# Kernel optimization log

Measured on AMD Instinct MI355X. Metric: run time of the kernel, lower is better.

Reference implementation:

```python
import jax, jax.numpy as jnp
import numpy as np

B, N = 128, 2048
DX = 10.0 / 2048.0   # X / N
DT = 5.0e-4          # CFL-consistent timestep


def f_real(u):
    # f(u) = 0.5*u*(3 - u^2) + (300/12)*u^2*(3/4 - 2u + 3/2 u^2 - 1/4 u^4)
    u2 = u * u
    return 0.5 * u * (3.0 - u2) + 25.0 * u2 * (0.75 - 2.0 * u + 1.5 * u2 - 0.25 * u2 * u2)


def dfdu_abs(u):
    # f_real is elementwise, so grad of the sum gives the elementwise derivative,
    # matching torch.autograd.grad(f, u, grad_outputs=ones_like(f))
    return jnp.abs(jax.grad(lambda uu: jnp.sum(f_real(uu)))(u))


def setup_inputs() -> dict:
    key = jax.random.key(0)
    init = jax.random.uniform(key, (B, N), dtype=jnp.float32)  # u in [0,1]
    return {"init": init, "stepnum": 500}


def reference(init, stepnum):
    lam = jnp.float32(DT / DX)

    def step(u_old, _):
        f = f_real(u_old)                      # [B, N]
        a = dfdu_abs(u_old)                    # |f'(u)|, [B, N]
        # local Lax-Friedrichs flux: max over the (j, j+1) pair
        alpha = jnp.maximum(a[:, :-1], a[:, 1:])  # [B, N-1]
        f_half = 0.5 * (f[:, :-1] + f[:, 1:]) - 0.5 * alpha * (u_old[:, 1:] - u_old[:, :-1])
        interior = u_old[:, 1:-1] - lam * (f_half[:, 1:] - f_half[:, :-1])  # [B, N-2]
        # boundary: u[:,0]=u[:,1], u[:,N-1]=u[:,N-2]
        u = jnp.concatenate([interior[:, :1], interior, interior[:, -1:]], axis=1)
        return u, u

    _, traj = jax.lax.scan(step, init, None, length=stepnum - 1)  # [stepnum-1, B, N]
    return jnp.concatenate([init[None], traj], axis=0)            # [stepnum, B, N]
```

## Files before the change

kernel.cpp:

```cpp
#include <hip/hip_runtime.h>

#define NPTS 2048
#define TPB  768
#define CAP  1536

typedef float v2f __attribute__((ext_vector_type(2)));

#define EDGE_BARRIER() do {                                   \
    asm volatile("s_waitcnt lgkmcnt(0)" ::: "memory");        \
    __builtin_amdgcn_s_barrier();                             \
    asm volatile("" ::: "memory");                            \
} while (0)

__device__ __forceinline__ v2f s2(float x) { v2f v; v.x = x; v.y = x; return v; }

__device__ __forceinline__ v2f fma2(v2f a, v2f b, v2f c) {
#if __has_builtin(__builtin_elementwise_fma)
    return __builtin_elementwise_fma(a, b, c);
#else
    v2f r; r.x = fmaf(a.x, b.x, c.x); r.y = fmaf(a.y, b.y, c.y); return r;
#endif
}

__device__ __forceinline__ void eval_gp2(v2f u, v2f& g, v2f& p) {
    const v2f uu = u * u;
    v2f gg = fma2(uu, s2(-3.125f), s2(18.75f));
    gg = fma2(u, gg, s2(-25.25f));
    gg = fma2(u, gg, s2(9.375f));
    gg = fma2(u, gg, s2(0.75f));
    g = u * gg;
    v2f pp = fma2(uu, s2(-37.5f), s2(150.0f));
    pp = fma2(u, pp, s2(-151.5f));
    pp = fma2(u, pp, s2(37.5f));
    p = fma2(u, pp, s2(1.5f));
}

__global__ __launch_bounds__(TPB) void lxf_split(
    const float* __restrict__ init, float* __restrict__ out,
    int nbatch, int nsteps)
{
    __shared__ float UL[2][TPB];
    __shared__ float UR[2][TPB];

    const int blk = blockIdx.x;
    const int r   = blk >> 1;
    const int h   = blk & 1;
    const int tid = threadIdx.x;
    const int c0  = 2 * tid;
    const int gb  = h ? 512 : 0;
    const size_t rowoff = (size_t)r * NPTS;
    const float lam = 0.1024f;

    const bool st  = h ? (c0 >= 512) : (c0 < 1024);
    const bool bcL = (h == 0) && (tid == 0);
    const bool bcR = (h == 1) && (tid == TPB - 1);
    const int  tl  = (tid == 0)       ? 0   : tid - 1;
    const int  tr  = (tid == TPB - 1) ? tid : tid + 1;
    const int dist = h ? (509 - c0) : (c0 - 1025);

    v2f uv = *reinterpret_cast<const v2f*>(init + rowoff + gb + c0);
    v2f gv, pv;
    eval_gp2(uv, gv, pv);

    if (st) *reinterpret_cast<v2f*>(out + rowoff + gb + c0) = uv;

    UL[0][tid] = uv.x;
    UR[0][tid] = uv.y;
    EDGE_BARRIER();

    const size_t stride = (size_t)nbatch * NPTS;
    float* dstw = out + rowoff + gb + c0;

#define STEP(CUR, NXT) do {                                              \
    dstw += stride;                                                      \
    if (dist <= rem) {                                                   \
        v2f h2; h2.x = UR[CUR][tl]; h2.y = UL[CUR][tr];      \
        v2f gh, ph;                                                      \
        eval_gp2(h2, gh, ph);                                            \
        const float aL = fmaxf(fabsf(ph.x), fabsf(pv.x));                \
        const float aM = fmaxf(fabsf(pv.x), fabsf(pv.y));                \
        const float aR = fmaxf(fabsf(pv.y), fabsf(ph.y));                \
        const float fhL = fmaf(-0.5f * aL, uv.x - h2.x, gh.x + gv.x);    \
        const float fhM = fmaf(-0.5f * aM, uv.y - uv.x, gv.x + gv.y);    \
        const float fhR = fmaf(-0.5f * aR, h2.y - uv.y, gv.y + gh.y);    \
        float n0 = fmaf(-lam, fhM - fhL, uv.x);                          \
        float n1 = fmaf(-lam, fhR - fhM, uv.y);                          \
        if (bcL) n0 = n1;                           \
        if (bcR) n1 = n0;                           \
        uv.x = n0; uv.y = n1;                                            \
        eval_gp2(uv, gv, pv);                                            \
        UL[NXT][tid] = n0;                                               \
        UR[NXT][tid] = n1;                                               \
        if (st) *reinterpret_cast<v2f*>(dstw) = uv;                      \
    }                                                                    \
    --rem;                                                               \
    EDGE_BARRIER();                                                      \
} while (0)

    const int S  = nsteps - 1;
    int rem = S - 1;
    const int P2 = S >> 1;
    for (int i = 0; i < P2; ++i) {
        STEP(0, 1);
        STEP(1, 0);
    }
    if (S & 1) STEP(0, 1);
#undef STEP
}

extern "C" void kernel_launch(void* const* d_in, const int* in_sizes, int n_in,
                              void* d_out, int out_size, void* d_ws, size_t ws_size,
                              hipStream_t stream) {
    const float* init = (const float*)d_in[0];
    float* out = (float*)d_out;

    const int nbatch = in_sizes[0] / NPTS;
    const int nsteps = out_size / in_sizes[0];

    hipLaunchKernelGGL(lxf_split, dim3(2 * nbatch), dim3(TPB), 0, stream,
                       init, out, nbatch, nsteps);
}
```

Baseline: 177.8 us.

## Fuse two time steps per barrier using halo-of-two and shared f/f' values

Each thread now reads a two-point halo from both neighbours and advances two time steps per barrier, halving the number of block-wide barriers. Neighbours' f and |f'| values are shared through LDS alongside u, so halo cells are not re-evaluated. The cost is redundant recomputation of the intermediate step at the halo, three times the LDS traffic, and more registers per thread. Boundary handling for the intermediate step, and a tail for odd step counts, are added.

```diff
diff --git a/kernel.cpp b/kernel.cpp
--- a/kernel.cpp
+++ b/kernel.cpp
@@ -2,7 +2,6 @@
 
 #define NPTS 2048
 #define TPB  768
-#define CAP  1536
 
 typedef float v2f __attribute__((ext_vector_type(2)));
 
@@ -39,8 +38,9 @@
     const float* __restrict__ init, float* __restrict__ out,
     int nbatch, int nsteps)
 {
-    __shared__ float UL[2][TPB];
-    __shared__ float UR[2][TPB];
+    __shared__ v2f Us[2][TPB];
+    __shared__ v2f Gs[2][TPB];
+    __shared__ v2f Ps[2][TPB];
 
     const int blk = blockIdx.x;
     const int r   = blk >> 1;
@@ -64,48 +64,95 @@
 
     if (st) *reinterpret_cast<v2f*>(out + rowoff + gb + c0) = uv;
 
-    UL[0][tid] = uv.x;
-    UR[0][tid] = uv.y;
+    Us[0][tid] = uv; Gs[0][tid] = gv; Ps[0][tid] = pv;
     EDGE_BARRIER();
 
     const size_t stride = (size_t)nbatch * NPTS;
     float* dstw = out + rowoff + gb + c0;
 
-#define STEP(CUR, NXT) do {                                              \
-    dstw += stride;                                                      \
-    if (dist <= rem) {                                                   \
-        v2f h2; h2.x = UR[CUR][tl]; h2.y = UL[CUR][tr];      \
-        v2f gh, ph;                                                      \
-        eval_gp2(h2, gh, ph);                                            \
-        const float aL = fmaxf(fabsf(ph.x), fabsf(pv.x));                \
-        const float aM = fmaxf(fabsf(pv.x), fabsf(pv.y));                \
-        const float aR = fmaxf(fabsf(pv.y), fabsf(ph.y));                \
-        const float fhL = fmaf(-0.5f * aL, uv.x - h2.x, gh.x + gv.x);    \
-        const float fhM = fmaf(-0.5f * aM, uv.y - uv.x, gv.x + gv.y);    \
-        const float fhR = fmaf(-0.5f * aR, h2.y - uv.y, gv.y + gh.y);    \
-        float n0 = fmaf(-lam, fhM - fhL, uv.x);                          \
-        float n1 = fmaf(-lam, fhR - fhM, uv.y);                          \
-        if (bcL) n0 = n1;                           \
-        if (bcR) n1 = n0;                           \
-        uv.x = n0; uv.y = n1;                                            \
-        eval_gp2(uv, gv, pv);                                            \
-        UL[NXT][tid] = n0;                                               \
-        UR[NXT][tid] = n1;                                               \
-        if (st) *reinterpret_cast<v2f*>(dstw) = uv;                      \
-    }                                                                    \
-    --rem;                                                               \
-    EDGE_BARRIER();                                                      \
+#define FLUX(gl, gr, pl, pr, ul, ur) \
+    fmaf(-0.5f * fmaxf(fabsf(pl), fabsf(pr)), (ur) - (ul), (gl) + (gr))
+
+#define SUPER(CUR, NXT) do {                                               \
+    dstw += 2 * stride;                                                    \
+    if (dist <= rem) {                                                     \
+        const v2f uLp = Us[CUR][tl], gLp = Gs[CUR][tl], pLp = Ps[CUR][tl]; \
+        const v2f uRp = Us[CUR][tr], gRp = Gs[CUR][tr], pRp = Ps[CUR][tr]; \
+        float yu[6], yg[6], yp[6];                                         \
+        yu[0]=uLp.x; yu[1]=uLp.y; yu[2]=uv.x; yu[3]=uv.y; yu[4]=uRp.x; yu[5]=uRp.y; \
+        yg[0]=gLp.x; yg[1]=gLp.y; yg[2]=gv.x; yg[3]=gv.y; yg[4]=gRp.x; yg[5]=gRp.y; \
+        yp[0]=pLp.x; yp[1]=pLp.y; yp[2]=pv.x; yp[3]=pv.y; yp[4]=pRp.x; yp[5]=pRp.y; \
+        if (tid == 0) {                                                    \
+            yu[0]=uv.x; yu[1]=uv.x; yg[0]=gv.x; yg[1]=gv.x;                \
+            yp[0]=pv.x; yp[1]=pv.x;                                        \
+        }                                                                  \
+        if (tid == TPB - 1) {                                              \
+            yu[4]=uv.y; yu[5]=uv.y; yg[4]=gv.y; yg[5]=gv.y;                \
+            yp[4]=pv.y; yp[5]=pv.y;                                        \
+        }                                                                  \
+                                    \
+        float F[5];                                                        \
+        _Pragma("unroll")                                                  \
+        for (int j = 0; j < 5; ++j)                                        \
+            F[j] = FLUX(yg[j], yg[j+1], yp[j], yp[j+1], yu[j], yu[j+1]);   \
+        float z0 = fmaf(-lam, F[1] - F[0], yu[1]);                         \
+        float z1 = fmaf(-lam, F[2] - F[1], yu[2]);                         \
+        float z2 = fmaf(-lam, F[3] - F[2], yu[3]);                         \
+        float z3 = fmaf(-lam, F[4] - F[3], yu[4]);                         \
+        if (bcL) { z1 = z2; z0 = z1; }        \
+        if (bcR) { z2 = z1; z3 = z2; }        \
+        if (st) { v2f o; o.x = z1; o.y = z2;                               \
+                  *reinterpret_cast<v2f*>(dstw - stride) = o; }            \
+                                    \
+        v2f za; za.x = z0; za.y = z1;                                      \
+        v2f zb; zb.x = z2; zb.y = z3;                                      \
+        v2f gza, pza, gzb, pzb;                                            \
+        eval_gp2(za, gza, pza);                                            \
+        eval_gp2(zb, gzb, pzb);                                            \
+        const float G0 = FLUX(gza.x, gza.y, pza.x, pza.y, z0, z1);         \
+        const float G1 = FLUX(gza.y, gzb.x, pza.y, pzb.x, z1, z2);         \
+        const float G2 = FLUX(gzb.x, gzb.y, pzb.x, pzb.y, z2, z3);         \
+        float w0 = fmaf(-lam, G1 - G0, z1);                                \
+        float w1 = fmaf(-lam, G2 - G1, z2);                                \
+        if (bcL) w0 = w1;                                                  \
+        if (bcR) w1 = w0;                                                  \
+        uv.x = w0; uv.y = w1;                                              \
+        eval_gp2(uv, gv, pv);                                              \
+        Us[NXT][tid] = uv; Gs[NXT][tid] = gv; Ps[NXT][tid] = pv;           \
+        if (st) *reinterpret_cast<v2f*>(dstw) = uv;                        \
+    }                                                                      \
+    rem -= 2;                                                              \
+    EDGE_BARRIER();                                                        \
 } while (0)
 
     const int S  = nsteps - 1;
-    int rem = S - 1;
     const int P2 = S >> 1;
-    for (int i = 0; i < P2; ++i) {
-        STEP(0, 1);
-        STEP(1, 0);
+    int rem = S;
+    for (int i = 0; i < P2 / 2; ++i) {
+        SUPER(0, 1);
+        SUPER(1, 0);
     }
-    if (S & 1) STEP(0, 1);
-#undef STEP
+    if (P2 & 1) SUPER(0, 1);
+    const int fin = P2 & 1;
+
+    if (S & 1) {
+        dstw += stride;
+        float uL = Us[fin][tl].y, gL = Gs[fin][tl].y, pL = Ps[fin][tl].y;
+        float uR = Us[fin][tr].x, gR = Gs[fin][tr].x, pR = Ps[fin][tr].x;
+        if (tid == 0)       { uL = uv.x; gL = gv.x; pL = pv.x; }
+        if (tid == TPB - 1) { uR = uv.y; gR = gv.y; pR = pv.y; }
+        const float fhL = FLUX(gL, gv.x, pL, pv.x, uL, uv.x);
+        const float fhM = FLUX(gv.x, gv.y, pv.x, pv.y, uv.x, uv.y);
+        const float fhR = FLUX(gv.y, gR, pv.y, pR, uv.y, uR);
+        float n0 = fmaf(-lam, fhM - fhL, uv.x);
+        float n1 = fmaf(-lam, fhR - fhM, uv.y);
+        if (bcL) n0 = n1;
+        if (bcR) n1 = n0;
+        if (st) { v2f o; o.x = n0; o.y = n1;
+                  *reinterpret_cast<v2f*>(dstw) = o; }
+    }
+#undef SUPER
+#undef FLUX
 }
 
 extern "C" void kernel_launch(void* const* d_in, const int* in_sizes, int n_in,
```

Result: no change. 178.6 us (+0.4%).

## Process four points per thread and share edge flux terms through LDS

Applied to the files above, without the earlier changes.

Each thread now owns four consecutive grid points instead of two, so the block shrinks from 768 to 384 threads while covering the same 1536-point window. Edge threads publish their u, f and |f'| values to shared memory, so neighbours no longer re-evaluate the flux polynomials for halo points. Loads and stores widen to 4-float vectors. In exchange there is more LDS traffic per step (three arrays) and more serial arithmetic per thread inside the barrier-bound 500-step loop.

```diff
diff --git a/kernel.cpp b/kernel.cpp
--- a/kernel.cpp
+++ b/kernel.cpp
@@ -1,10 +1,10 @@
 #include <hip/hip_runtime.h>
 
 #define NPTS 2048
-#define TPB  768
-#define CAP  1536
+#define TPB  384
 
 typedef float v2f __attribute__((ext_vector_type(2)));
+typedef float v4f __attribute__((ext_vector_type(4)));
 
 #define EDGE_BARRIER() do {                                   \
     asm volatile("s_waitcnt lgkmcnt(0)" ::: "memory");        \
@@ -35,18 +35,22 @@
     p = fma2(u, pp, s2(1.5f));
 }
 
+#define FLUX(gl, gr, pl, pr, ul, ur) \
+    fmaf(-0.5f * fmaxf(fabsf(pl), fabsf(pr)), (ur) - (ul), (gl) + (gr))
+
 __global__ __launch_bounds__(TPB) void lxf_split(
     const float* __restrict__ init, float* __restrict__ out,
     int nbatch, int nsteps)
 {
-    __shared__ float UL[2][TPB];
-    __shared__ float UR[2][TPB];
+    __shared__ v2f EU[2][TPB];
+    __shared__ v2f EG[2][TPB];
+    __shared__ v2f EP[2][TPB];
 
     const int blk = blockIdx.x;
     const int r   = blk >> 1;
     const int h   = blk & 1;
     const int tid = threadIdx.x;
-    const int c0  = 2 * tid;
+    const int c0  = 4 * tid;
     const int gb  = h ? 512 : 0;
     const size_t rowoff = (size_t)r * NPTS;
     const float lam = 0.1024f;
@@ -56,16 +60,18 @@
     const bool bcR = (h == 1) && (tid == TPB - 1);
     const int  tl  = (tid == 0)       ? 0   : tid - 1;
     const int  tr  = (tid == TPB - 1) ? tid : tid + 1;
-    const int dist = h ? (509 - c0) : (c0 - 1025);
+    const int dist = h ? (507 - c0) : (c0 - 1025);
 
-    v2f uv = *reinterpret_cast<const v2f*>(init + rowoff + gb + c0);
-    v2f gv, pv;
-    eval_gp2(uv, gv, pv);
+    v4f a = *reinterpret_cast<const v4f*>(init + rowoff + gb + c0);
+    float s0 = a.x, s1 = a.y, s2v = a.z, s3 = a.w;
 
-    if (st) *reinterpret_cast<v2f*>(out + rowoff + gb + c0) = uv;
+    v2f ue; ue.x = s0; ue.y = s3;
+    v2f ge, pe;
+    eval_gp2(ue, ge, pe);
 
-    UL[0][tid] = uv.x;
-    UR[0][tid] = uv.y;
+    if (st) *reinterpret_cast<v4f*>(out + rowoff + gb + c0) = a;
+
+    EU[0][tid] = ue; EG[0][tid] = ge; EP[0][tid] = pe;
     EDGE_BARRIER();
 
     const size_t stride = (size_t)nbatch * NPTS;
@@ -74,24 +80,33 @@
 #define STEP(CUR, NXT) do {                                              \
     dstw += stride;                                                      \
     if (dist <= rem) {                                                   \
-        v2f h2; h2.x = UR[CUR][tl]; h2.y = UL[CUR][tr];      \
-        v2f gh, ph;                                                      \
-        eval_gp2(h2, gh, ph);                                            \
-        const float aL = fmaxf(fabsf(ph.x), fabsf(pv.x));                \
-        const float aM = fmaxf(fabsf(pv.x), fabsf(pv.y));                \
-        const float aR = fmaxf(fabsf(pv.y), fabsf(ph.y));                \
-        const float fhL = fmaf(-0.5f * aL, uv.x - h2.x, gh.x + gv.x);    \
-        const float fhM = fmaf(-0.5f * aM, uv.y - uv.x, gv.x + gv.y);    \
-        const float fhR = fmaf(-0.5f * aR, h2.y - uv.y, gv.y + gh.y);    \
-        float n0 = fmaf(-lam, fhM - fhL, uv.x);                          \
-        float n1 = fmaf(-lam, fhR - fhM, uv.y);                          \
+                                         \
+        float uL = EU[CUR][tl].y, gL = EG[CUR][tl].y, pL = EP[CUR][tl].y;\
+        float uR = EU[CUR][tr].x, gR = EG[CUR][tr].x, pR = EP[CUR][tr].x;\
+                    \
+        v2f ui; ui.x = s1; ui.y = s2v;                                   \
+        v2f gi, pi;                                                      \
+        eval_gp2(ui, gi, pi);                                            \
+        const float F1 = FLUX(ge.x, gi.x, pe.x, pi.x, s0, s1);           \
+        const float F2 = FLUX(gi.x, gi.y, pi.x, pi.y, s1, s2v);          \
+        const float F3 = FLUX(gi.y, ge.y, pi.y, pe.y, s2v, s3);          \
+        if (tid == 0)       { uL = s0; gL = ge.x; pL = pe.x; }           \
+        if (tid == TPB - 1) { uR = s3; gR = ge.y; pR = pe.y; }           \
+        const float F0 = FLUX(gL, ge.x, pL, pe.x, uL, s0);               \
+        const float F4 = FLUX(ge.y, gR, pe.y, pR, s3, uR);               \
+        float n0 = fmaf(-lam, F1 - F0, s0);                              \
+        float n1 = fmaf(-lam, F2 - F1, s1);                              \
+        float n2 = fmaf(-lam, F3 - F2, s2v);                             \
+        float n3 = fmaf(-lam, F4 - F3, s3);                              \
         if (bcL) n0 = n1;                           \
-        if (bcR) n1 = n0;                           \
-        uv.x = n0; uv.y = n1;                                            \
-        eval_gp2(uv, gv, pv);                                            \
-        UL[NXT][tid] = n0;                                               \
-        UR[NXT][tid] = n1;                                               \
-        if (st) *reinterpret_cast<v2f*>(dstw) = uv;                      \
+        if (bcR) n3 = n2;                           \
+        s0 = n0; s1 = n1; s2v = n2; s3 = n3;                             \
+              \
+        ue.x = n0; ue.y = n3;                                            \
+        eval_gp2(ue, ge, pe);                                            \
+        EU[NXT][tid] = ue; EG[NXT][tid] = ge; EP[NXT][tid] = pe;         \
+        if (st) { v4f w; w.x = n0; w.y = n1; w.z = n2; w.w = n3;         \
+                  *reinterpret_cast<v4f*>(dstw) = w; }                   \
     }                                                                    \
     --rem;                                                               \
     EDGE_BARRIER();                                                      \
```

Result: slower. 193.1 us (+8.6%).

## Use wavefront-local halo shuffles with overlapping tiles, sync every 64 steps

Applied to the files above, without the earlier changes.

Replaces the per-step block-wide barrier and LDS exchange with a wave-local scheme. Each wavefront owns 256 cells with 64-cell halos on each side, and neighbours are exchanged via lane shuffles. The block resynchronises through shared memory only every 64 steps. This removes roughly 500 barriers per launch at the cost of redundant halo computation, 4 cells per thread, and shuffles of u, g and p each step.

```diff
diff --git a/kernel.cpp b/kernel.cpp
--- a/kernel.cpp
+++ b/kernel.cpp
@@ -1,16 +1,11 @@
 #include <hip/hip_runtime.h>
 
-#define NPTS 2048
-#define TPB  768
-#define CAP  1536
+#define NPTS   2048
+#define TPB    768
+#define BCELLS 1536
 
+typedef float v4f __attribute__((ext_vector_type(4)));
 typedef float v2f __attribute__((ext_vector_type(2)));
-
-#define EDGE_BARRIER() do {                                   \
-    asm volatile("s_waitcnt lgkmcnt(0)" ::: "memory");        \
-    __builtin_amdgcn_s_barrier();                             \
-    asm volatile("" ::: "memory");                            \
-} while (0)
 
 __device__ __forceinline__ v2f s2(float x) { v2f v; v.x = x; v.y = x; return v; }
 
@@ -35,77 +30,109 @@
     p = fma2(u, pp, s2(1.5f));
 }
 
-__global__ __launch_bounds__(TPB) void lxf_split(
+#define FLUX(gl, gr, pl, pr, ul, ur) \
+    fmaf(-0.5f * fmaxf(fabsf(pl), fabsf(pr)), (ur) - (ul), (gl) + (gr))
+
+__global__ __launch_bounds__(TPB) void lxf_wave(
     const float* __restrict__ init, float* __restrict__ out,
     int nbatch, int nsteps)
 {
-    __shared__ float UL[2][TPB];
-    __shared__ float UR[2][TPB];
+    __shared__ float UALL[BCELLS];
 
-    const int blk = blockIdx.x;
-    const int r   = blk >> 1;
-    const int h   = blk & 1;
-    const int tid = threadIdx.x;
-    const int c0  = 2 * tid;
-    const int gb  = h ? 512 : 0;
+    const int blk  = blockIdx.x;
+    const int r    = blk >> 1;
+    const int h    = blk & 1;
+    const int tid  = threadIdx.x;
+    const int w    = tid >> 6;
+    const int lane = tid & 63;
+    const int goff = h ? 512 : 0;
     const size_t rowoff = (size_t)r * NPTS;
     const float lam = 0.1024f;
 
-    const bool st  = h ? (c0 >= 512) : (c0 < 1024);
-    const bool bcL = (h == 0) && (tid == 0);
-    const bool bcR = (h == 1) && (tid == TPB - 1);
-    const int  tl  = (tid == 0)       ? 0   : tid - 1;
-    const int  tr  = (tid == TPB - 1) ? tid : tid + 1;
-    const int dist = h ? (509 - c0) : (c0 - 1025);
+    const int base = (w == 0) ? 0 : ((w == 11) ? 1280 : 128 * w - 64);
+    const int c0   = base + 4 * lane;
 
-    v2f uv = *reinterpret_cast<const v2f*>(init + rowoff + gb + c0);
-    v2f gv, pv;
-    eval_gp2(uv, gv, pv);
+    const int  ol0      = (w == 0) ? 0 : ((w == 11) ? 32 : 16);
+    const bool own_lane = (lane >= ol0) && (lane < ol0 + 32);
+    const bool stmask   = own_lane && (h ? (w >= 4) : (w <= 7));
 
-    if (st) *reinterpret_cast<v2f*>(out + rowoff + gb + c0) = uv;
+    const bool bcL = (h == 0) && (w == 0)  && (lane == 0);
+    const bool bcR = (h == 1) && (w == 11) && (lane == 63);
 
-    UL[0][tid] = uv.x;
-    UR[0][tid] = uv.y;
-    EDGE_BARRIER();
+    v4f uv = *reinterpret_cast<const v4f*>(init + rowoff + goff + c0);
+    float u0 = uv.x, u1 = uv.y, u2 = uv.z, u3 = uv.w;
+    float g0, g1, g2, g3, p0, p1, p2, p3;
+    {
+        v2f a, ga, pa, b, gb2, pb2;
+        a.x = u0; a.y = u1; eval_gp2(a, ga, pa);
+        b.x = u2; b.y = u3; eval_gp2(b, gb2, pb2);
+        g0 = ga.x; g1 = ga.y; g2 = gb2.x; g3 = gb2.y;
+        p0 = pa.x; p1 = pa.y; p2 = pb2.x; p3 = pb2.y;
+    }
+
+    float* dst = out + rowoff + goff + c0;
+    if (stmask) *reinterpret_cast<v4f*>(dst) = uv;
 
     const size_t stride = (size_t)nbatch * NPTS;
-    float* dstw = out + rowoff + gb + c0;
+    const int S = nsteps - 1;
+    int done = 0;
 
-#define STEP(CUR, NXT) do {                                              \
-    dstw += stride;                                                      \
-    if (dist <= rem) {                                                   \
-        v2f h2; h2.x = UR[CUR][tl]; h2.y = UL[CUR][tr];      \
-        v2f gh, ph;                                                      \
-        eval_gp2(h2, gh, ph);                                            \
-        const float aL = fmaxf(fabsf(ph.x), fabsf(pv.x));                \
-        const float aM = fmaxf(fabsf(pv.x), fabsf(pv.y));                \
-        const float aR = fmaxf(fabsf(pv.y), fabsf(ph.y));                \
-        const float fhL = fmaf(-0.5f * aL, uv.x - h2.x, gh.x + gv.x);    \
-        const float fhM = fmaf(-0.5f * aM, uv.y - uv.x, gv.x + gv.y);    \
-        const float fhR = fmaf(-0.5f * aR, h2.y - uv.y, gv.y + gh.y);    \
-        float n0 = fmaf(-lam, fhM - fhL, uv.x);                          \
-        float n1 = fmaf(-lam, fhR - fhM, uv.y);                          \
-        if (bcL) n0 = n1;                           \
-        if (bcR) n1 = n0;                           \
-        uv.x = n0; uv.y = n1;                                            \
-        eval_gp2(uv, gv, pv);                                            \
-        UL[NXT][tid] = n0;                                               \
-        UR[NXT][tid] = n1;                                               \
-        if (st) *reinterpret_cast<v2f*>(dstw) = uv;                      \
-    }                                                                    \
-    --rem;                                                               \
-    EDGE_BARRIER();                                                      \
-} while (0)
+    while (done < S) {
+        int Kr = S - done;
+        if (Kr > 64) Kr = 64;
 
-    const int S  = nsteps - 1;
-    int rem = S - 1;
-    const int P2 = S >> 1;
-    for (int i = 0; i < P2; ++i) {
-        STEP(0, 1);
-        STEP(1, 0);
+        for (int k = 0; k < Kr; ++k) {
+            dst += stride;
+            const float uL = __shfl_up(u3, 1);
+            const float gL = __shfl_up(g3, 1);
+            const float pL = __shfl_up(p3, 1);
+            const float uR = __shfl_down(u0, 1);
+            const float gR = __shfl_down(g0, 1);
+            const float pR = __shfl_down(p0, 1);
+
+            const float F0 = FLUX(gL, g0, pL, p0, uL, u0);
+            const float F1 = FLUX(g0, g1, p0, p1, u0, u1);
+            const float F2 = FLUX(g1, g2, p1, p2, u1, u2);
+            const float F3 = FLUX(g2, g3, p2, p3, u2, u3);
+            const float F4 = FLUX(g3, gR, p3, pR, u3, uR);
+
+            float n0 = fmaf(-lam, F1 - F0, u0);
+            float n1 = fmaf(-lam, F2 - F1, u1);
+            float n2 = fmaf(-lam, F3 - F2, u2);
+            float n3 = fmaf(-lam, F4 - F3, u3);
+            n0 = bcL ? n1 : n0;
+            n3 = bcR ? n2 : n3;
+            u0 = n0; u1 = n1; u2 = n2; u3 = n3;
+
+            v2f a, ga, pa, b, gb2, pb2;
+            a.x = u0; a.y = u1; eval_gp2(a, ga, pa);
+            b.x = u2; b.y = u3; eval_gp2(b, gb2, pb2);
+            g0 = ga.x; g1 = ga.y; g2 = gb2.x; g3 = gb2.y;
+            p0 = pa.x; p1 = pa.y; p2 = pb2.x; p3 = pb2.y;
+
+            if (stmask) {
+                v4f wv; wv.x = u0; wv.y = u1; wv.z = u2; wv.w = u3;
+                *reinterpret_cast<v4f*>(dst) = wv;
+            }
+        }
+        done += Kr;
+
+        if (done < S) {
+            __syncthreads();
+            if (own_lane) {
+                v4f wv; wv.x = u0; wv.y = u1; wv.z = u2; wv.w = u3;
+                *reinterpret_cast<v4f*>(&UALL[c0]) = wv;
+            }
+            __syncthreads();
+            v4f rv = *reinterpret_cast<const v4f*>(&UALL[c0]);
+            u0 = rv.x; u1 = rv.y; u2 = rv.z; u3 = rv.w;
+            v2f a, ga, pa, b, gb2, pb2;
+            a.x = u0; a.y = u1; eval_gp2(a, ga, pa);
+            b.x = u2; b.y = u3; eval_gp2(b, gb2, pb2);
+            g0 = ga.x; g1 = ga.y; g2 = gb2.x; g3 = gb2.y;
+            p0 = pa.x; p1 = pa.y; p2 = pb2.x; p3 = pb2.y;
+        }
     }
-    if (S & 1) STEP(0, 1);
-#undef STEP
 }
 
 extern "C" void kernel_launch(void* const* d_in, const int* in_sizes, int n_in,
@@ -117,6 +144,6 @@
     const int nbatch = in_sizes[0] / NPTS;
     const int nsteps = out_size / in_sizes[0];
 
-    hipLaunchKernelGGL(lxf_split, dim3(2 * nbatch), dim3(TPB), 0, stream,
+    hipLaunchKernelGGL(lxf_wave, dim3(2 * nbatch), dim3(TPB), 0, stream,
                        init, out, nbatch, nsteps);
 }
```

Result: slower. 233.0 us (+31.1%).
